# Kernel optimization log

Hardware: AMD Instinct MI355X
Metric: run time of the kernel (lower is better)

## Reference

```python
import jax, jax.numpy as jnp
import numpy as np

VOCAB = 30001  # vocab_size + 1
EMB = 64
CHAR = 50
RNN = 128
TAGS = 9
B, T = 256, 512
D_IN = EMB + CHAR  # 114


def lstm_scan(x, Wx, Wh, b):
    # x: [T, B, D]; Keras LSTM gate order i, f, g(c), o; sigmoid/tanh activations.
    Bsz = x.shape[1]
    H = Wh.shape[0]
    def step(carry, xt):
        h, c = carry
        z = xt @ Wx + h @ Wh + b  # [B, 4H]
        i, f, g, o = jnp.split(z, 4, axis=-1)
        c = jax.nn.sigmoid(f) * c + jax.nn.sigmoid(i) * jnp.tanh(g)
        h = jax.nn.sigmoid(o) * jnp.tanh(c)
        return (h, c), h
    init = (jnp.zeros((Bsz, H), x.dtype), jnp.zeros((Bsz, H), x.dtype))
    _, hs = jax.lax.scan(step, init, x)
    return hs  # [T, B, H]


def crf_log_likelihood(logits, labels, lengths, trans):
    # logits: [B,T,K]; labels: [B,T] int; lengths: [B] int; trans: [K,K]
    Bsz, Tlen, K = logits.shape
    mask = (jnp.arange(Tlen)[None, :] < lengths[:, None]).astype(logits.dtype)  # [B,T]
    # gold path score: unary + pairwise transition terms
    unary = jnp.take_along_axis(logits, labels[..., None], axis=-1)[..., 0]  # [B,T]
    unary_score = jnp.sum(unary * mask, axis=1)
    binary = trans[labels[:, :-1], labels[:, 1:]]  # [B,T-1]
    binary_score = jnp.sum(binary * mask[:, 1:], axis=1)
    seq_score = unary_score + binary_score
    # forward algorithm (log-domain scan over time)
    logits_t = jnp.transpose(logits, (1, 0, 2))  # [T,B,K]
    mask_t = jnp.transpose(mask[:, 1:])          # [T-1,B]
    def step(alpha, inp):
        logit_t, m = inp
        new = jax.nn.logsumexp(alpha[:, :, None] + trans[None], axis=1) + logit_t
        alpha = jnp.where(m[:, None] > 0, new, alpha)
        return alpha, None
    alpha, _ = jax.lax.scan(step, logits_t[0], (logits_t[1:], mask_t))
    log_norm = jax.nn.logsumexp(alpha, axis=1)
    log_norm = jnp.where(lengths > 0, log_norm, jnp.zeros_like(log_norm))
    return seq_score - log_norm


def setup_inputs() -> dict:
    key = jax.random.key(0)
    ks = jax.random.split(key, 12)
    inputs = jax.random.randint(ks[0], (B, T), 0, 30000, dtype=jnp.int32)
    char_embeddings = jax.random.normal(ks[1], (B, T, CHAR), dtype=jnp.float32)
    labels = jax.random.randint(ks[2], (B, T), 0, TAGS, dtype=jnp.int32)
    E = 0.1 * jax.random.normal(ks[3], (VOCAB, EMB), dtype=jnp.float32)
    s_in = 1.0 / np.sqrt(D_IN)
    s_h = 1.0 / np.sqrt(RNN)
    Wx_f = s_in * jax.random.normal(ks[4], (D_IN, 4 * RNN), dtype=jnp.float32)
    Wh_f = s_h * jax.random.normal(ks[5], (RNN, 4 * RNN), dtype=jnp.float32)
    b_f = jnp.zeros((4 * RNN,), jnp.float32)
    Wx_b = s_in * jax.random.normal(ks[6], (D_IN, 4 * RNN), dtype=jnp.float32)
    Wh_b = s_h * jax.random.normal(ks[7], (RNN, 4 * RNN), dtype=jnp.float32)
    b_b = jnp.zeros((4 * RNN,), jnp.float32)
    Wd = (1.0 / np.sqrt(2 * RNN)) * jax.random.normal(ks[8], (2 * RNN, TAGS), dtype=jnp.float32)
    bd = jnp.zeros((TAGS,), jnp.float32)
    transition = jax.random.uniform(ks[9], (TAGS, TAGS), dtype=jnp.float32)
    return {"inputs": inputs, "char_embeddings": char_embeddings, "labels": labels,
            "E": E, "Wx_f": Wx_f, "Wh_f": Wh_f, "b_f": b_f,
            "Wx_b": Wx_b, "Wh_b": Wh_b, "b_b": b_b,
            "Wd": Wd, "bd": bd, "transition": transition}


def reference(inputs, char_embeddings, labels, E, Wx_f, Wh_f, b_f, Wx_b, Wh_b, b_b, Wd, bd, transition):
    emb = E[inputs]                                      # [B,T,64]
    x = jnp.concatenate([emb, char_embeddings], axis=2)  # [B,T,114]
    xt = jnp.transpose(x, (1, 0, 2))                     # [T,B,114]
    h_f = lstm_scan(xt, Wx_f, Wh_f, b_f)                 # [T,B,128]
    h_b = lstm_scan(xt[::-1], Wx_b, Wh_b, b_b)[::-1]     # [T,B,128]
    out = jnp.concatenate([h_f, h_b], axis=-1)           # [T,B,256]
    logits = jnp.transpose(out, (1, 0, 2)) @ Wd + bd     # [B,T,9]
    lengths = jnp.sum((labels != 0).astype(jnp.int32), axis=1)
    log_likelihood = crf_log_likelihood(logits, labels, lengths, transition)
    return log_likelihood, transition
```

## Files before the change

kernel.cpp:

```cpp
#include <hip/hip_runtime.h>

#define BB   256
#define TT   512
#define EMBD 64
#define CHARD 50
#define DIN  114
#define RNN  128
#define NG   512
#define TAGS 9

typedef __bf16 bf16x8 __attribute__((ext_vector_type(8)));
typedef float  f32x4  __attribute__((ext_vector_type(4)));
typedef unsigned int u32x2 __attribute__((ext_vector_type(2)));

static __device__ __forceinline__ unsigned short f2bf(float f) {
  unsigned int u = __float_as_uint(f);
  unsigned int r = (u + 0x7FFFu + ((u >> 16) & 1u)) >> 16;
  return (unsigned short)r;
}
static __device__ __forceinline__ void gl_lds16(const void* g, void* l) {
  __builtin_amdgcn_global_load_lds(
      (const __attribute__((address_space(1))) unsigned int*)g,
      (__attribute__((address_space(3))) unsigned int*)l, 16, 0, 0);
}

__global__ void k_build_x(const int* __restrict__ inp, const float* __restrict__ ch,
                          const float* __restrict__ E, unsigned short* __restrict__ x) {
  int idx = blockIdx.x * 256 + threadIdx.x;
  int k   = idx & 127;
  int row = idx >> 7;
  float v;
  if (k < EMBD)      v = E[inp[row] * EMBD + k];
  else if (k < DIN)  v = ch[row * CHARD + (k - EMBD)];
  else               v = 0.f;
  x[idx] = f2bf(v);
}

__global__ void k_prep_w(const float* __restrict__ Wx_f, const float* __restrict__ Wh_f,
                         const float* __restrict__ Wx_b, const float* __restrict__ Wh_b,
                         const float* __restrict__ Wd,
                         unsigned short* __restrict__ WxT, unsigned short* __restrict__ WhT,
                         unsigned short* __restrict__ WdT) {
  if (blockIdx.x == 512) {
    for (int i = threadIdx.x; i < 16 * 256; i += 256) {
      int n = i >> 8, k = i & 255;
      WdT[i] = (n < TAGS) ? f2bf(Wd[k * TAGS + n]) : (unsigned short)0;
    }
    return;
  }
  int idx = blockIdx.x * 256 + threadIdx.x;
  int dir = idx >> 16;
  int rem = idx & 65535;
  int n   = rem >> 7;
  int kk  = rem & 127;
  const float* Wx = dir ? Wx_b : Wx_f;
  const float* Wh = dir ? Wh_b : Wh_f;
  WxT[idx] = (kk < DIN) ? f2bf(Wx[kk * NG + n]) : (unsigned short)0;
  WhT[idx] = f2bf(Wh[kk * NG + n]);
}

__global__ void k_lengths(const int* __restrict__ labels, int* __restrict__ lengths) {
  int b = blockIdx.x, lane = threadIdx.x;
  int cnt = 0;
  for (int t = lane; t < TT; t += 64) cnt += (labels[b * TT + t] != 0);
  for (int o = 32; o > 0; o >>= 1) cnt += __shfl_down(cnt, o);
  if (lane == 0) lengths[b] = cnt;
}

__global__ __launch_bounds__(512, 2) void k_fused(
    const unsigned short* __restrict__ x,
    const unsigned short* __restrict__ WxT,
    const unsigned short* __restrict__ WhT,
    const float* __restrict__ b_f, const float* __restrict__ b_b,
    const unsigned short* __restrict__ zcons, unsigned short* __restrict__ zprod,
    unsigned short* __restrict__ hseq, float* __restrict__ cbuf,
    int lstm_n, int s0, int s1, int first, int zs0, int znsteps)
{
  __shared__ __align__(16) char LDS[32768];
  const int tid = threadIdx.x, w = tid >> 6, l = tid & 63;
  const int lq = l & 15, lg = l >> 4;

  if ((int)blockIdx.x < lstm_n) {
    const int wg = blockIdx.x, dir = wg >> 5, rg = wg & 31, b0 = rg * 8;
    const unsigned short* WhD = WhT + dir * (NG * 128);
    unsigned short* hout = hseq + (size_t)dir * ((size_t)BB * TT * 128);
    char* ring = LDS;

    bf16x8 wh[4][4];
    #pragma unroll
    for (int g = 0; g < 4; ++g)
      #pragma unroll
      for (int kt = 0; kt < 4; ++kt)
        wh[g][kt] = *reinterpret_cast<const bf16x8*>(
            WhD + (g * RNN + w * 16 + lq) * 128 + kt * 32 + lg * 8);

    const int row7 = l & 7;
    int ro[4];
    #pragma unroll
    for (int kt = 0; kt < 4; ++kt)
      ro[kt] = (row7 * 16 + (((kt * 4) + lg) ^ row7)) * 16;

    int wo[2], rowr[2];
    #pragma unroll
    for (int rr = 0; rr < 2; ++rr) {
      rowr[rr] = (lg & 1) * 4 + (lg >> 1) * 2 + rr;
      int unit = rowr[rr] * 16 + ((w * 2 + (lq >> 3)) ^ rowr[rr]);
      wo[rr] = unit * 16 + (lq & 7) * 2;
    }
    const int hidden = w * 16 + lq;

    if (tid < 128) {
      int row = tid >> 4, h16 = tid & 15;
      int unit = row * 16 + (h16 ^ row);
      if (first) {
        *reinterpret_cast<f32x4*>(ring + 7 * 2048 + unit * 16) = f32x4{0.f, 0.f, 0.f, 0.f};
      } else {
        int tprev = dir ? (TT - s0) : (s0 - 1);
        bf16x8 v = *reinterpret_cast<const bf16x8*>(
            hout + ((size_t)(b0 + row) * TT + tprev) * 128 + h16 * 8);
        *reinterpret_cast<bf16x8*>(ring + 7 * 2048 + unit * 16) = v;
      }
    }
    float c[2];
    #pragma unroll
    for (int rr = 0; rr < 2; ++rr)
      c[rr] = first ? 0.f : cbuf[(size_t)(dir * BB + b0 + rowr[rr]) * RNN + hidden];
    __syncthreads();

    const unsigned short* zQ = zcons +
        (size_t)(((dir * 32 + rg) * 8 + w) * 2 + (lg & 1)) * 256 + lq * 4;
    u32x2 zA[4], zB[4];
    if (lg < 2) {
      #pragma unroll
      for (int g = 0; g < 4; ++g) zA[g] = *reinterpret_cast<const u32x2*>(zQ + g * 64);
      const unsigned short* zp1 = zQ + (size_t)((s0 + 1 < s1) ? 1 : 0) * 262144;
      #pragma unroll
      for (int g = 0; g < 4; ++g) zB[g] = *reinterpret_cast<const u32x2*>(zp1 + g * 64);
    }

    auto gather = [&](int sp) {
      int h16 = tid & 15, tc = (tid >> 4) & 3, row = tid >> 6;
      int ss = sp + tc, t = dir ? (TT - 1 - ss) : ss;
      bf16x8 v = *reinterpret_cast<const bf16x8*>(
          ring + (ss & 7) * 2048 + (row * 16 + (h16 ^ row)) * 16);
      *reinterpret_cast<bf16x8*>(hout + ((size_t)(b0 + row) * TT + t) * 128 + h16 * 8) = v;
    };

    for (int s = s0; s < s1; ++s) {
      f32x4 acc[4];
      #pragma unroll
      for (int g = 0; g < 4; ++g) {
        unsigned int lo = zA[g][0], hi = zA[g][1];
        f32x4 zv = f32x4{__uint_as_float(lo << 16), __uint_as_float(lo & 0xffff0000u),
                         __uint_as_float(hi << 16), __uint_as_float(hi & 0xffff0000u)};
        acc[g] = (lg < 2) ? zv : f32x4{0.f, 0.f, 0.f, 0.f};
      }
      {
        #pragma unroll
        for (int g = 0; g < 4; ++g) zA[g] = zB[g];
        int sn = (s + 2 < s1) ? (s + 2) : (s1 - 1);
        if (lg < 2) {
          const unsigned short* zp = zQ + (size_t)(sn - s0) * 262144;
          #pragma unroll
          for (int g = 0; g < 4; ++g) zB[g] = *reinterpret_cast<const u32x2*>(zp + g * 64);
        }
      }

      const char* rb = ring + ((s - 1) & 7) * 2048;
      bf16x8 hf[4];
      #pragma unroll
      for (int kt = 0; kt < 4; ++kt)
        hf[kt] = *reinterpret_cast<const bf16x8*>(rb + ro[kt]);
      #pragma unroll
      for (int kt = 0; kt < 4; ++kt)
        #pragma unroll
        for (int g = 0; g < 4; ++g)
          acc[g] = __builtin_amdgcn_mfma_f32_16x16x32_bf16(hf[kt], wh[g][kt], acc[g], 0, 0, 0);

      if ((s & 3) == 0 && s > s0) gather(s - 4);

      float sw_[4][2];
      #pragma unroll
      for (int g = 0; g < 4; ++g)
        #pragma unroll
        for (int rr = 0; rr < 2; ++rr) {
          float d = acc[g][2 + rr], sv = acc[g][2 + rr];
          asm volatile("v_permlane32_swap_b32 %0, %1" : "+v"(d), "+v"(sv));
          sw_[g][rr] = d;
        }

      char* wslot = ring + (s & 7) * 2048;
      #pragma unroll
      for (int rr = 0; rr < 2; ++rr) {
        float zi = (lg < 2) ? acc[0][rr] : sw_[0][rr];
        float zf = (lg < 2) ? acc[1][rr] : sw_[1][rr];
        float zg = (lg < 2) ? acc[2][rr] : sw_[2][rr];
        float zo = (lg < 2) ? acc[3][rr] : sw_[3][rr];
        zi = fminf(20.f, fmaxf(-20.f, zi));
        zf = fminf(20.f, fmaxf(-20.f, zf));
        zg = fminf(20.f, fmaxf(-20.f, zg));
        zo = fminf(20.f, fmaxf(-20.f, zo));
        float ei = __expf(-zi), ef = __expf(-zf), eo = __expf(-zo);
        float g2 = __expf(2.f * zg);
        float P   = (1.f + ei) * (g2 + 1.f);
        float efp = 1.f + ef;
        float cn  = (c[rr] * P + efp * (g2 - 1.f)) * __builtin_amdgcn_rcpf(efp * P);
        c[rr] = cn;
        float cc = fminf(20.f, fmaxf(-20.f, cn));
        float ec = __expf(2.f * cc);
        float hn = (ec - 1.f) * __builtin_amdgcn_rcpf((1.f + eo) * (ec + 1.f));
        *reinterpret_cast<unsigned short*>(wslot + wo[rr]) = f2bf(hn);
      }
      __builtin_amdgcn_sched_barrier(0);
      asm volatile("s_waitcnt lgkmcnt(0)" ::: "memory");
      __builtin_amdgcn_s_barrier();
      __builtin_amdgcn_sched_barrier(0);
    }

    gather(s1 - 4);
    #pragma unroll
    for (int rr = 0; rr < 2; ++rr)
      cbuf[(size_t)(dir * BB + b0 + rowr[rr]) * RNN + hidden] = c[rr];
  } else {
    if (znsteps <= 0) return;
    const int TCHN = znsteps >> 4;
    const int zb = blockIdx.x - lstm_n;
    const int per = 16 * TCHN;
    const int dir = zb / per;
    const int rem = zb % per;
    const int rg2 = rem / TCHN, tch = rem % TCHN;
    const int b0p = rg2 * 16;
    const int sb  = zs0 + tch * 16;

    const unsigned short* WxD = WxT + dir * (NG * 128);
    const float* bias = dir ? b_b : b_f;
    unsigned short* xr = (unsigned short*)LDS;

    bf16x8 wx[4][4];
    float  bs[4];
    #pragma unroll
    for (int g = 0; g < 4; ++g) {
      int n = g * RNN + w * 16 + lq;
      bs[g] = bias[n];
      #pragma unroll
      for (int kt = 0; kt < 4; ++kt)
        wx[g][kt] = *reinterpret_cast<const bf16x8*>(WxD + n * 128 + kt * 32 + lg * 8);
    }

    auto stage = [&](int ci) {
      int buf = ci & 1;
      #pragma unroll
      for (int jj = 0; jj < 2; ++jj) {
        int idx = w * 2 + jj, sc = idx >> 2, kt = idx & 3;
        int s = sb + ci * 4 + sc;
        int t = dir ? (TT - 1 - s) : s;
        gl_lds16(x + ((size_t)(b0p + lq) * TT + t) * 128 + kt * 32 + lg * 8,
                 xr + buf * 8192 + sc * 2048 + kt * 512);
      }
    };

    stage(0);
    for (int ci = 0; ci < 4; ++ci) {
      __syncthreads();
      if (ci < 3) stage(ci + 1);
      int buf = ci & 1;
      #pragma unroll
      for (int sc = 0; sc < 4; ++sc) {
        int s = sb + ci * 4 + sc;
        bf16x8 xf[4];
        #pragma unroll
        for (int kt = 0; kt < 4; ++kt)
          xf[kt] = *reinterpret_cast<const bf16x8*>(xr + buf * 8192 + sc * 2048 + kt * 512 + l * 8);
        f32x4 acc[4];
        #pragma unroll
        for (int g = 0; g < 4; ++g) acc[g] = f32x4{bs[g], bs[g], bs[g], bs[g]};
        #pragma unroll
        for (int kt = 0; kt < 4; ++kt)
          #pragma unroll
          for (int g = 0; g < 4; ++g)
            acc[g] = __builtin_amdgcn_mfma_f32_16x16x32_bf16(xf[kt], wx[g][kt], acc[g], 0, 0, 0);
        unsigned short* zp = zprod + (size_t)(s - zs0) * 262144 +
            (size_t)(((dir * 32 + rg2 * 2 + (lg >> 1)) * 8 + w) * 2 + (lg & 1)) * 256 + lq * 4;
        #pragma unroll
        for (int g = 0; g < 4; ++g) {
          ushort4 v;
          v.x = f2bf(acc[g][0]); v.y = f2bf(acc[g][1]);
          v.z = f2bf(acc[g][2]); v.w = f2bf(acc[g][3]);
          *reinterpret_cast<ushort4*>(zp + g * 64) = v;
        }
      }
    }
  }
}

__global__ __launch_bounds__(256) void k_logits(const unsigned short* __restrict__ hseq,
                                                const unsigned short* __restrict__ WdT,
                                                const float* __restrict__ bd,
                                                float* __restrict__ logits,
                                                float* __restrict__ euk) {
  __shared__ __align__(16) unsigned short xt[2][16384];
  const int tid = threadIdx.x, wv = tid >> 6, l = tid & 63;
  const int lq = l & 15, lg = l >> 4;
  const size_t HS = (size_t)BB * TT * 128;

  bf16x8 wb[8];
  #pragma unroll
  for (int kt = 0; kt < 8; ++kt)
    wb[kt] = *reinterpret_cast<const bf16x8*>(WdT + lq * 256 + kt * 32 + lg * 8);
  float bdv = (lq < TAGS) ? bd[lq] : 0.f;

  auto stage = [&](int it, int buf) {
    int bt0 = blockIdx.x * 256 + it * 64;
    #pragma unroll
    for (int i = 0; i < 8; ++i) {
      int v = tid + i * 256;
      int g = v ^ ((v >> 5) & 7);
      int row = g >> 5, cu = g & 31;
      const unsigned short* src = (cu < 16)
          ? hseq + (size_t)(bt0 + row) * 128 + cu * 8
          : hseq + HS + (size_t)(bt0 + row) * 128 + (cu - 16) * 8;
      gl_lds16(src, &xt[buf][(i * 256 + wv * 64) * 8]);
    }
  };

  stage(0, 0);
  for (int it = 0; it < 4; ++it) {
    __syncthreads();
    if (it < 3) stage(it + 1, (it + 1) & 1);
    int buf = it & 1;
    int bt0 = blockIdx.x * 256 + it * 64;
    int r0 = wv * 16;
    bf16x8 af[8];
    #pragma unroll
    for (int kt = 0; kt < 8; ++kt) {
      int u = (r0 + lq) * 32 + kt * 4 + lg;
      af[kt] = *reinterpret_cast<const bf16x8*>(&xt[buf][(u ^ ((u >> 5) & 7)) * 8]);
    }
    f32x4 acc = f32x4{bdv, bdv, bdv, bdv};
    #pragma unroll
    for (int kt = 0; kt < 8; ++kt)
      acc = __builtin_amdgcn_mfma_f32_16x16x32_bf16(af[kt], wb[kt], acc, 0, 0, 0);
    float mr[4];
    #pragma unroll
    for (int r = 0; r < 4; ++r) {
      float v = (lq < TAGS) ? acc[r] : -1e30f;
      #pragma unroll
      for (int o = 1; o < 16; o <<= 1) v = fmaxf(v, __shfl_xor(v, o, 16));
      mr[r] = v;
    }
    #pragma unroll
    for (int r = 0; r < 4; ++r) {
      int rowi = bt0 + r0 + lg * 4 + r;
      if (lq < TAGS) logits[(size_t)rowi * TAGS + lq] = acc[r];
      if (lq < 12) {
        float val = (lq < TAGS) ? __expf(acc[r] - mr[r]) : ((lq == TAGS) ? mr[r] : 0.f);
        euk[(size_t)rowi * 12 + lq] = val;
      }
    }
  }
}

__global__ void k_score(const float* __restrict__ logits, const int* __restrict__ labels,
                        const int* __restrict__ lengths, const float* __restrict__ trans,
                        float* __restrict__ scbuf) {
  int b = blockIdx.x, lane = threadIdx.x;
  int len = lengths[b];
  const float* lg = logits + (size_t)b * TT * TAGS;
  const int*   lab = labels + b * TT;
  float sc = 0.f;
  for (int t = lane; t < TT; t += 64) {
    if (t < len) {
      sc += lg[t * TAGS + lab[t]];
      if (t >= 1) sc += trans[lab[t - 1] * TAGS + lab[t]];
    }
  }
  for (int o = 32; o > 0; o >>= 1) sc += __shfl_down(sc, o);
  if (lane == 0) scbuf[b] = sc;
}

__global__ __launch_bounds__(256, 1) void k_crf2(const float* __restrict__ euk,
                                                 const float* __restrict__ scbuf,
                                                 const int* __restrict__ lengths,
                                                 const float* __restrict__ trans,
                                                 float* __restrict__ out) {
  const int wv = threadIdx.x >> 6, lane = threadIdx.x & 63;
  const int b = blockIdx.x * 4 + wv;
  const float* ep = euk + (size_t)b * TT * 12;
  const int len = lengths[b];
  const int lim = (len < TT) ? len : TT;

  float Et[81];
  #pragma unroll
  for (int i = 0; i < 81; ++i) Et[i] = __expf(trans[i]);

  float P[81];
  float Ks = 0.f;
  int   E2 = 0;

  const int t0 = 1 + lane * 8;
  auto rec = [&](int t) { int tl = (t < TT) ? t : (TT - 1); return ep + (size_t)tl * 12; };

  const float* p0 = rec(t0);
  float4 A0 = *(const float4*)p0, A1 = *(const float4*)(p0 + 4), A2 = *(const float4*)(p0 + 8);
  const float* p1 = rec(t0 + 1);
  float4 B0 = *(const float4*)p1, B1 = *(const float4*)(p1 + 4), B2 = *(const float4*)(p1 + 8);

  {
    float eu[9] = {A0.x, A0.y, A0.z, A0.w, A1.x, A1.y, A1.z, A1.w, A2.x};
    bool upd = t0 < lim;
    #pragma unroll
    for (int i = 0; i < 9; ++i)
      #pragma unroll
      for (int j = 0; j < 9; ++j)
        P[i * 9 + j] = upd ? Et[i * 9 + j] * eu[j] : ((i == j) ? 1.f : 0.f);
    Ks += upd ? A2.y : 0.f;
    A0 = B0; A1 = B1; A2 = B2;
    const float* pn = rec(t0 + 2);
    B0 = *(const float4*)pn; B1 = *(const float4*)(pn + 4); B2 = *(const float4*)(pn + 8);
  }

  for (int s = 1; s < 8; ++s) {
    float eu[9] = {A0.x, A0.y, A0.z, A0.w, A1.x, A1.y, A1.z, A1.w, A2.x};
    float mt = A2.y;
    bool upd = (t0 + s) < lim;
    A0 = B0; A1 = B1; A2 = B2;
    const float* pn = rec(t0 + s + 2);
    B0 = *(const float4*)pn; B1 = *(const float4*)(pn + 4); B2 = *(const float4*)(pn + 8);
    #pragma unroll
    for (int i = 0; i < 9; ++i) {
      float tmp[9];
      #pragma unroll
      for (int j = 0; j < 9; ++j) {
        float a = P[i * 9 + 0] * Et[0 * 9 + j];
        #pragma unroll
        for (int k = 1; k < 9; ++k) a = fmaf(P[i * 9 + k], Et[k * 9 + j], a);
        tmp[j] = a * eu[j];
      }
      #pragma unroll
      for (int j = 0; j < 9; ++j) P[i * 9 + j] = upd ? tmp[j] : P[i * 9 + j];
    }
    Ks += upd ? mt : 0.f;
  }

  {
    float m = P[0];
    #pragma unroll
    for (int e = 1; e < 81; ++e) m = fmaxf(m, P[e]);
    int ex; frexpf(m, &ex);
    #pragma unroll
    for (int e = 0; e < 81; ++e) P[e] = ldexpf(P[e], -ex);
    E2 += ex;
  }

  for (int d = 0; d < 6; ++d) {
    int msk = 1 << d;
    float Q[81];
    #pragma unroll
    for (int e = 0; e < 81; ++e) Q[e] = __shfl_xor(P[e], msk);
    int   E2p = __shfl_xor(E2, msk);
    float Ksp = __shfl_xor(Ks, msk);
    bool late = (lane & msk) != 0;
    #pragma unroll
    for (int e = 0; e < 81; ++e) {
      float a = P[e], q = Q[e];
      P[e] = late ? q : a;
      Q[e] = late ? a : q;
    }
    #pragma unroll
    for (int i = 0; i < 9; ++i) {
      float tmp[9];
      #pragma unroll
      for (int j = 0; j < 9; ++j) {
        float a = P[i * 9 + 0] * Q[0 * 9 + j];
        #pragma unroll
        for (int k = 1; k < 9; ++k) a = fmaf(P[i * 9 + k], Q[k * 9 + j], a);
        tmp[j] = a;
      }
      #pragma unroll
      for (int j = 0; j < 9; ++j) P[i * 9 + j] = tmp[j];
    }
    E2 += E2p; Ks += Ksp;
    float m = P[0];
    #pragma unroll
    for (int e = 1; e < 81; ++e) m = fmaxf(m, P[e]);
    int ex; frexpf(m, &ex);
    #pragma unroll
    for (int e = 0; e < 81; ++e) P[e] = ldexpf(P[e], -ex);
    E2 += ex;
  }

  float4 z0 = *(const float4*)ep, z1 = *(const float4*)(ep + 4), z2 = *(const float4*)(ep + 8);
  float eu0[9] = {z0.x, z0.y, z0.z, z0.w, z1.x, z1.y, z1.z, z1.w, z2.x};
  float alpha[9];
  #pragma unroll
  for (int j = 0; j < 9; ++j) {
    float a = eu0[0] * P[0 * 9 + j];
    #pragma unroll
    for (int i = 1; i < 9; ++i) a = fmaf(eu0[i], P[i * 9 + j], a);
    alpha[j] = a;
  }
  float S = ((alpha[0] + alpha[1]) + (alpha[2] + alpha[3])) +
            ((alpha[4] + alpha[5]) + (alpha[6] + alpha[7])) + alpha[8];
  float ln = logf(S) + (float)E2 * 0.69314718056f + Ks + z2.y;
  if (lane == 0) out[b] = (len > 0) ? (scbuf[b] - ln) : 0.f;
}

__global__ void k_copy_trans(const float* __restrict__ trans, float* __restrict__ out) {
  int i = threadIdx.x;
  if (i < TAGS * TAGS) out[BB + i] = trans[i];
}

extern "C" void kernel_launch(void* const* d_in, const int* in_sizes, int n_in,
                              void* d_out, int out_size, void* d_ws, size_t ws_size,
                              hipStream_t stream) {
  const int*   inp    = (const int*)d_in[0];
  const float* ch     = (const float*)d_in[1];
  const int*   labels = (const int*)d_in[2];
  const float* E      = (const float*)d_in[3];
  const float* Wx_f   = (const float*)d_in[4];
  const float* Wh_f   = (const float*)d_in[5];
  const float* b_f    = (const float*)d_in[6];
  const float* Wx_b   = (const float*)d_in[7];
  const float* Wh_b   = (const float*)d_in[8];
  const float* b_b    = (const float*)d_in[9];
  const float* Wd     = (const float*)d_in[10];
  const float* bd     = (const float*)d_in[11];
  const float* trans  = (const float*)d_in[12];
  float* out = (float*)d_out;

  unsigned short* x    = (unsigned short*)d_ws;
  unsigned short* hseq = x + (size_t)BB * TT * 128;
  unsigned short* WxT  = hseq + (size_t)2 * BB * TT * 128;
  unsigned short* WhT  = WxT + 2 * NG * 128;
  unsigned short* WdT  = WhT + 2 * NG * 128;
  float* logits        = (float*)(WdT + 16 * 256);
  float* euk           = logits + (size_t)BB * TT * TAGS;
  float* cbuf          = euk + (size_t)BB * TT * 12;
  float* scbuf         = cbuf + (size_t)2 * BB * RNN;
  int*   lengths       = (int*)(scbuf + BB);
  unsigned short* zbuf = (unsigned short*)(lengths + 256);

  const size_t zoff = (size_t)((char*)zbuf - (char*)d_ws);
  int NP = 4;
  const int cands[4] = {4, 8, 16, 32};
  for (int i = 0; i < 4; ++i) {
    NP = cands[i];
    if (zoff + 2ull * (size_t)(TT / NP) * 524288ull <= ws_size) break;
  }
  const int L = TT / NP;
  const size_t zsl = (size_t)L * 262144;

  k_build_x<<<(BB * TT * 128) / 256, 256, 0, stream>>>(inp, ch, E, x);
  k_prep_w<<<513, 256, 0, stream>>>(Wx_f, Wh_f, Wx_b, Wh_b, Wd, WxT, WhT, WdT);
  k_lengths<<<BB, 64, 0, stream>>>(labels, lengths);

  k_fused<<<2 * 16 * (L / 16), 512, 0, stream>>>(x, WxT, WhT, b_f, b_b,
                                                 zbuf, zbuf, hseq, cbuf,
                                                 0, 0, 0, 1, 0, L);
  for (int p = 0; p < NP; ++p) {
    int nz = (p + 1 < NP) ? 2 * 16 * (L / 16) : 0;
    k_fused<<<64 + nz, 512, 0, stream>>>(
        x, WxT, WhT, b_f, b_b,
        zbuf + (size_t)(p & 1) * zsl,
        zbuf + (size_t)((p + 1) & 1) * zsl,
        hseq, cbuf,
        64, p * L, (p + 1) * L, (p == 0) ? 1 : 0, (p + 1) * L, nz ? L : 0);
  }

  k_logits<<<(BB * TT) / 256, 256, 0, stream>>>(hseq, WdT, bd, logits, euk);
  k_score<<<BB, 64, 0, stream>>>(logits, labels, lengths, trans, scbuf);
  k_crf2<<<BB / 4, 256, 0, stream>>>(euk, scbuf, lengths, trans, out);
  k_copy_trans<<<1, 128, 0, stream>>>(trans, out);
}
```

Baseline: 605.6 us.

## Add producer wavefronts that prefetch gate inputs into LDS and write hidden states

Grows the LSTM workgroup from 8 to 10 wavefronts. The two extra producer waves stage the precomputed input-projection gates into a double-buffered LDS region with global_load_lds, and they also copy hidden states from the LDS ring out to global memory. The 8 compute waves no longer issue global loads or stores in the serial recurrence loop and instead read gate inputs from LDS. In exchange the workgroup uses more LDS and registers, the producer waves must match the compute waves' barrier count every step, and the launch bounds change may cap registers per thread.

```diff
diff --git a/kernel.cpp b/kernel.cpp
--- a/kernel.cpp
+++ b/kernel.cpp
@@ -67,7 +67,7 @@
   if (lane == 0) lengths[b] = cnt;
 }
 
-__global__ __launch_bounds__(512, 2) void k_fused(
+__global__ __launch_bounds__(640, 5) void k_fused(
     const unsigned short* __restrict__ x,
     const unsigned short* __restrict__ WxT,
     const unsigned short* __restrict__ WhT,
@@ -76,7 +76,7 @@
     unsigned short* __restrict__ hseq, float* __restrict__ cbuf,
     int lstm_n, int s0, int s1, int first, int zs0, int znsteps)
 {
-  __shared__ __align__(16) char LDS[32768];
+  __shared__ __align__(16) char LDS[49152];
   const int tid = threadIdx.x, w = tid >> 6, l = tid & 63;
   const int lq = l & 15, lg = l >> 4;
 
@@ -85,29 +85,33 @@
     const unsigned short* WhD = WhT + dir * (NG * 128);
     unsigned short* hout = hseq + (size_t)dir * ((size_t)BB * TT * 128);
     char* ring = LDS;
+    char* zst  = LDS + 16384;
 
     bf16x8 wh[4][4];
-    #pragma unroll
-    for (int g = 0; g < 4; ++g)
+    int ro[4], wo[2], rowr[2], hidden = 0;
+    float c[2] = {0.f, 0.f};
+    if (w < 8) {
+      #pragma unroll
+      for (int g = 0; g < 4; ++g)
+        #pragma unroll
+        for (int kt = 0; kt < 4; ++kt)
+          wh[g][kt] = *reinterpret_cast<const bf16x8*>(
+              WhD + (g * RNN + w * 16 + lq) * 128 + kt * 32 + lg * 8);
+      const int row7 = l & 7;
       #pragma unroll
       for (int kt = 0; kt < 4; ++kt)
-        wh[g][kt] = *reinterpret_cast<const bf16x8*>(
-            WhD + (g * RNN + w * 16 + lq) * 128 + kt * 32 + lg * 8);
-
-    const int row7 = l & 7;
-    int ro[4];
-    #pragma unroll
-    for (int kt = 0; kt < 4; ++kt)
-      ro[kt] = (row7 * 16 + (((kt * 4) + lg) ^ row7)) * 16;
-
-    int wo[2], rowr[2];
-    #pragma unroll
-    for (int rr = 0; rr < 2; ++rr) {
-      rowr[rr] = (lg & 1) * 4 + (lg >> 1) * 2 + rr;
-      int unit = rowr[rr] * 16 + ((w * 2 + (lq >> 3)) ^ rowr[rr]);
-      wo[rr] = unit * 16 + (lq & 7) * 2;
-    }
-    const int hidden = w * 16 + lq;
+        ro[kt] = (row7 * 16 + (((kt * 4) + lg) ^ row7)) * 16;
+      #pragma unroll
+      for (int rr = 0; rr < 2; ++rr) {
+        rowr[rr] = (lg & 1) * 4 + (lg >> 1) * 2 + rr;
+        int unit = rowr[rr] * 16 + ((w * 2 + (lq >> 3)) ^ rowr[rr]);
+        wo[rr] = unit * 16 + (lq & 7) * 2;
+      }
+      hidden = w * 16 + lq;
+      #pragma unroll
+      for (int rr = 0; rr < 2; ++rr)
+        c[rr] = first ? 0.f : cbuf[(size_t)(dir * BB + b0 + rowr[rr]) * RNN + hidden];
+    }
 
     if (tid < 128) {
       int row = tid >> 4, h16 = tid & 15;
@@ -121,106 +125,128 @@
         *reinterpret_cast<bf16x8*>(ring + 7 * 2048 + unit * 16) = v;
       }
     }
-    float c[2];
-    #pragma unroll
-    for (int rr = 0; rr < 2; ++rr)
-      c[rr] = first ? 0.f : cbuf[(size_t)(dir * BB + b0 + rowr[rr]) * RNN + hidden];
+
+    if (w >= 8) {
+      int sw = w - 8;
+      const unsigned short* src = zcons + (size_t)sw * 262144 + (size_t)(dir * 32 + rg) * 4096;
+      char* dst = zst + sw * 8192;
+      #pragma unroll
+      for (int i = 0; i < 8; ++i)
+        gl_lds16(src + i * 512 + l * 8, dst + i * 1024 + l * 16);
+      asm volatile("s_waitcnt vmcnt(0)" ::: "memory");
+    }
     __syncthreads();
 
-    const unsigned short* zQ = zcons +
-        (size_t)(((dir * 32 + rg) * 8 + w) * 2 + (lg & 1)) * 256 + lq * 4;
-    u32x2 zA[4], zB[4];
-    if (lg < 2) {
-      #pragma unroll
-      for (int g = 0; g < 4; ++g) zA[g] = *reinterpret_cast<const u32x2*>(zQ + g * 64);
-      const unsigned short* zp1 = zQ + (size_t)((s0 + 1 < s1) ? 1 : 0) * 262144;
-      #pragma unroll
-      for (int g = 0; g < 4; ++g) zB[g] = *reinterpret_cast<const u32x2*>(zp1 + g * 64);
-    }
-
-    auto gather = [&](int sp) {
-      int h16 = tid & 15, tc = (tid >> 4) & 3, row = tid >> 6;
-      int ss = sp + tc, t = dir ? (TT - 1 - ss) : ss;
-      bf16x8 v = *reinterpret_cast<const bf16x8*>(
-          ring + (ss & 7) * 2048 + (row * 16 + (h16 ^ row)) * 16);
-      *reinterpret_cast<bf16x8*>(hout + ((size_t)(b0 + row) * TT + t) * 128 + h16 * 8) = v;
-    };
-
-    for (int s = s0; s < s1; ++s) {
-      f32x4 acc[4];
-      #pragma unroll
-      for (int g = 0; g < 4; ++g) {
-        unsigned int lo = zA[g][0], hi = zA[g][1];
-        f32x4 zv = f32x4{__uint_as_float(lo << 16), __uint_as_float(lo & 0xffff0000u),
-                         __uint_as_float(hi << 16), __uint_as_float(hi & 0xffff0000u)};
-        acc[g] = (lg < 2) ? zv : f32x4{0.f, 0.f, 0.f, 0.f};
+    if (w < 8) {
+      for (int s = s0; s < s1; ++s) {
+        int ls = s - s0;
+        const char* zls = zst + ((ls >> 1) & 1) * 16384 + (ls & 1) * 8192 +
+                          (w * 2 + (lg & 1)) * 512 + lq * 8;
+        u32x2 zr[4];
+        #pragma unroll
+        for (int g = 0; g < 4; ++g)
+          zr[g] = *reinterpret_cast<const u32x2*>(zls + g * 128);
+
+        f32x4 acc[4];
+        #pragma unroll
+        for (int g = 0; g < 4; ++g) {
+          unsigned int lo = zr[g][0], hi = zr[g][1];
+          f32x4 zv = f32x4{__uint_as_float(lo << 16), __uint_as_float(lo & 0xffff0000u),
+                           __uint_as_float(hi << 16), __uint_as_float(hi & 0xffff0000u)};
+          acc[g] = (lg < 2) ? zv : f32x4{0.f, 0.f, 0.f, 0.f};
+        }
+
+        const char* rb = ring + ((s - 1) & 7) * 2048;
+        bf16x8 hf[4];
+        #pragma unroll
+        for (int kt = 0; kt < 4; ++kt)
+          hf[kt] = *reinterpret_cast<const bf16x8*>(rb + ro[kt]);
+        #pragma unroll
+        for (int kt = 0; kt < 4; ++kt)
+          #pragma unroll
+          for (int g = 0; g < 4; ++g)
+            acc[g] = __builtin_amdgcn_mfma_f32_16x16x32_bf16(hf[kt], wh[g][kt], acc[g], 0, 0, 0);
+
+        float sw_[4][2];
+        #pragma unroll
+        for (int g = 0; g < 4; ++g)
+          #pragma unroll
+          for (int rr = 0; rr < 2; ++rr) {
+            float d = acc[g][2 + rr], sv = acc[g][2 + rr];
+            asm volatile("v_permlane32_swap_b32 %0, %1" : "+v"(d), "+v"(sv));
+            sw_[g][rr] = d;
+          }
+
+        char* wslot = ring + (s & 7) * 2048;
+        #pragma unroll
+        for (int rr = 0; rr < 2; ++rr) {
+          float zi = (lg < 2) ? acc[0][rr] : sw_[0][rr];
+          float zf = (lg < 2) ? acc[1][rr] : sw_[1][rr];
+          float zg = (lg < 2) ? acc[2][rr] : sw_[2][rr];
+          float zo = (lg < 2) ? acc[3][rr] : sw_[3][rr];
+          zi = fminf(20.f, fmaxf(-20.f, zi));
+          zf = fminf(20.f, fmaxf(-20.f, zf));
+          zg = fminf(20.f, fmaxf(-20.f, zg));
+          zo = fminf(20.f, fmaxf(-20.f, zo));
+          float ei = __expf(-zi), ef = __expf(-zf), eo = __expf(-zo);
+          float g2 = __expf(2.f * zg);
+          float P   = (1.f + ei) * (g2 + 1.f);
+          float efp = 1.f + ef;
+          float cn  = (c[rr] * P + efp * (g2 - 1.f)) * __builtin_amdgcn_rcpf(efp * P);
+          c[rr] = cn;
+          float cc = fminf(20.f, fmaxf(-20.f, cn));
+          float ec = __expf(2.f * cc);
+          float hn = (ec - 1.f) * __builtin_amdgcn_rcpf((1.f + eo) * (ec + 1.f));
+          *reinterpret_cast<unsigned short*>(wslot + wo[rr]) = f2bf(hn);
+        }
+        __builtin_amdgcn_sched_barrier(0);
+        asm volatile("s_waitcnt lgkmcnt(0)" ::: "memory");
+        __builtin_amdgcn_s_barrier();
+        __builtin_amdgcn_sched_barrier(0);
+      }
+      #pragma unroll
+      for (int rr = 0; rr < 2; ++rr)
+        cbuf[(size_t)(dir * BB + b0 + rowr[rr]) * RNN + hidden] = c[rr];
+    } else {
+      const int sw = w - 8;
+      for (int s = s0; s < s1; ++s) {
+        int ls = s - s0;
+        if ((ls & 1) == 0 && s + 2 < s1) {
+          int st = ls + 2 + sw;
+          const unsigned short* src = zcons + (size_t)st * 262144 + (size_t)(dir * 32 + rg) * 4096;
+          char* dst = zst + (((ls >> 1) + 1) & 1) * 16384 + sw * 8192;
+          #pragma unroll
+          for (int i = 0; i < 8; ++i)
+            gl_lds16(src + i * 512 + l * 8, dst + i * 1024 + l * 16);
+        }
+        if ((s & 3) == 0 && s > s0) {
+          int lid = sw * 64 + l;
+          #pragma unroll
+          for (int j = 0; j < 4; ++j) {
+            int u = lid + j * 128;
+            int h16 = u & 15, tc = (u >> 4) & 3, row = u >> 6;
+            int ss = s - 4 + tc, t = dir ? (TT - 1 - ss) : ss;
+            bf16x8 v = *reinterpret_cast<const bf16x8*>(
+                ring + (ss & 7) * 2048 + (row * 16 + (h16 ^ row)) * 16);
+            *reinterpret_cast<bf16x8*>(hout + ((size_t)(b0 + row) * TT + t) * 128 + h16 * 8) = v;
+          }
+        }
+        if ((ls & 1) == 1) asm volatile("s_waitcnt vmcnt(0)" ::: "memory");
+        __builtin_amdgcn_s_barrier();
       }
       {
-        #pragma unroll
-        for (int g = 0; g < 4; ++g) zA[g] = zB[g];
-        int sn = (s + 2 < s1) ? (s + 2) : (s1 - 1);
-        if (lg < 2) {
-          const unsigned short* zp = zQ + (size_t)(sn - s0) * 262144;
-          #pragma unroll
-          for (int g = 0; g < 4; ++g) zB[g] = *reinterpret_cast<const u32x2*>(zp + g * 64);
+        int lid = sw * 64 + l;
+        #pragma unroll
+        for (int j = 0; j < 4; ++j) {
+          int u = lid + j * 128;
+          int h16 = u & 15, tc = (u >> 4) & 3, row = u >> 6;
+          int ss = s1 - 4 + tc, t = dir ? (TT - 1 - ss) : ss;
+          bf16x8 v = *reinterpret_cast<const bf16x8*>(
+              ring + (ss & 7) * 2048 + (row * 16 + (h16 ^ row)) * 16);
+          *reinterpret_cast<bf16x8*>(hout + ((size_t)(b0 + row) * TT + t) * 128 + h16 * 8) = v;
         }
       }
-
-      const char* rb = ring + ((s - 1) & 7) * 2048;
-      bf16x8 hf[4];
-      #pragma unroll
-      for (int kt = 0; kt < 4; ++kt)
-        hf[kt] = *reinterpret_cast<const bf16x8*>(rb + ro[kt]);
-      #pragma unroll
-      for (int kt = 0; kt < 4; ++kt)
-        #pragma unroll
-        for (int g = 0; g < 4; ++g)
-          acc[g] = __builtin_amdgcn_mfma_f32_16x16x32_bf16(hf[kt], wh[g][kt], acc[g], 0, 0, 0);
-
-      if ((s & 3) == 0 && s > s0) gather(s - 4);
-
-      float sw_[4][2];
-      #pragma unroll
-      for (int g = 0; g < 4; ++g)
-        #pragma unroll
-        for (int rr = 0; rr < 2; ++rr) {
-          float d = acc[g][2 + rr], sv = acc[g][2 + rr];
-          asm volatile("v_permlane32_swap_b32 %0, %1" : "+v"(d), "+v"(sv));
-          sw_[g][rr] = d;
-        }
-
-      char* wslot = ring + (s & 7) * 2048;
-      #pragma unroll
-      for (int rr = 0; rr < 2; ++rr) {
-        float zi = (lg < 2) ? acc[0][rr] : sw_[0][rr];
-        float zf = (lg < 2) ? acc[1][rr] : sw_[1][rr];
-        float zg = (lg < 2) ? acc[2][rr] : sw_[2][rr];
-        float zo = (lg < 2) ? acc[3][rr] : sw_[3][rr];
-        zi = fminf(20.f, fmaxf(-20.f, zi));
-        zf = fminf(20.f, fmaxf(-20.f, zf));
-        zg = fminf(20.f, fmaxf(-20.f, zg));
-        zo = fminf(20.f, fmaxf(-20.f, zo));
-        float ei = __expf(-zi), ef = __expf(-zf), eo = __expf(-zo);
-        float g2 = __expf(2.f * zg);
-        float P   = (1.f + ei) * (g2 + 1.f);
-        float efp = 1.f + ef;
-        float cn  = (c[rr] * P + efp * (g2 - 1.f)) * __builtin_amdgcn_rcpf(efp * P);
-        c[rr] = cn;
-        float cc = fminf(20.f, fmaxf(-20.f, cn));
-        float ec = __expf(2.f * cc);
-        float hn = (ec - 1.f) * __builtin_amdgcn_rcpf((1.f + eo) * (ec + 1.f));
-        *reinterpret_cast<unsigned short*>(wslot + wo[rr]) = f2bf(hn);
-      }
-      __builtin_amdgcn_sched_barrier(0);
-      asm volatile("s_waitcnt lgkmcnt(0)" ::: "memory");
-      __builtin_amdgcn_s_barrier();
-      __builtin_amdgcn_sched_barrier(0);
-    }
-
-    gather(s1 - 4);
-    #pragma unroll
-    for (int rr = 0; rr < 2; ++rr)
-      cbuf[(size_t)(dir * BB + b0 + rowr[rr]) * RNN + hidden] = c[rr];
+    }
   } else {
     if (znsteps <= 0) return;
     const int TCHN = znsteps >> 4;
@@ -238,16 +264,19 @@
 
     bf16x8 wx[4][4];
     float  bs[4];
-    #pragma unroll
-    for (int g = 0; g < 4; ++g) {
-      int n = g * RNN + w * 16 + lq;
-      bs[g] = bias[n];
-      #pragma unroll
-      for (int kt = 0; kt < 4; ++kt)
-        wx[g][kt] = *reinterpret_cast<const bf16x8*>(WxD + n * 128 + kt * 32 + lg * 8);
+    if (w < 8) {
+      #pragma unroll
+      for (int g = 0; g < 4; ++g) {
+        int n = g * RNN + w * 16 + lq;
+        bs[g] = bias[n];
+        #pragma unroll
+        for (int kt = 0; kt < 4; ++kt)
+          wx[g][kt] = *reinterpret_cast<const bf16x8*>(WxD + n * 128 + kt * 32 + lg * 8);
+      }
     }
 
     auto stage = [&](int ci) {
+      if (w >= 8) return;
       int buf = ci & 1;
       #pragma unroll
       for (int jj = 0; jj < 2; ++jj) {
@@ -263,30 +292,32 @@
     for (int ci = 0; ci < 4; ++ci) {
       __syncthreads();
       if (ci < 3) stage(ci + 1);
-      int buf = ci & 1;
-      #pragma unroll
-      for (int sc = 0; sc < 4; ++sc) {
-        int s = sb + ci * 4 + sc;
-        bf16x8 xf[4];
-        #pragma unroll
-        for (int kt = 0; kt < 4; ++kt)
-          xf[kt] = *reinterpret_cast<const bf16x8*>(xr + buf * 8192 + sc * 2048 + kt * 512 + l * 8);
-        f32x4 acc[4];
-        #pragma unroll
-        for (int g = 0; g < 4; ++g) acc[g] = f32x4{bs[g], bs[g], bs[g], bs[g]};
-        #pragma unroll
-        for (int kt = 0; kt < 4; ++kt)
-          #pragma unroll
-          for (int g = 0; g < 4; ++g)
-            acc[g] = __builtin_amdgcn_mfma_f32_16x16x32_bf16(xf[kt], wx[g][kt], acc[g], 0, 0, 0);
-        unsigned short* zp = zprod + (size_t)(s - zs0) * 262144 +
-            (size_t)(((dir * 32 + rg2 * 2 + (lg >> 1)) * 8 + w) * 2 + (lg & 1)) * 256 + lq * 4;
-        #pragma unroll
-        for (int g = 0; g < 4; ++g) {
-          ushort4 v;
-          v.x = f2bf(acc[g][0]); v.y = f2bf(acc[g][1]);
-          v.z = f2bf(acc[g][2]); v.w = f2bf(acc[g][3]);
-          *reinterpret_cast<ushort4*>(zp + g * 64) = v;
+      if (w < 8) {
+        int buf = ci & 1;
+        #pragma unroll
+        for (int sc = 0; sc < 4; ++sc) {
+          int s = sb + ci * 4 + sc;
+          bf16x8 xf[4];
+          #pragma unroll
+          for (int kt = 0; kt < 4; ++kt)
+            xf[kt] = *reinterpret_cast<const bf16x8*>(xr + buf * 8192 + sc * 2048 + kt * 512 + l * 8);
+          f32x4 acc[4];
+          #pragma unroll
+          for (int g = 0; g < 4; ++g) acc[g] = f32x4{bs[g], bs[g], bs[g], bs[g]};
+          #pragma unroll
+          for (int kt = 0; kt < 4; ++kt)
+            #pragma unroll
+            for (int g = 0; g < 4; ++g)
+              acc[g] = __builtin_amdgcn_mfma_f32_16x16x32_bf16(xf[kt], wx[g][kt], acc[g], 0, 0, 0);
+          unsigned short* zp = zprod + (size_t)(s - zs0) * 262144 +
+              (size_t)(((dir * 32 + rg2 * 2 + (lg >> 1)) * 8 + w) * 2 + (lg & 1)) * 256 + lq * 4;
+          #pragma unroll
+          for (int g = 0; g < 4; ++g) {
+            ushort4 v;
+            v.x = f2bf(acc[g][0]); v.y = f2bf(acc[g][1]);
+            v.z = f2bf(acc[g][2]); v.w = f2bf(acc[g][3]);
+            *reinterpret_cast<ushort4*>(zp + g * 64) = v;
+          }
         }
       }
     }
@@ -554,12 +585,12 @@
   k_prep_w<<<513, 256, 0, stream>>>(Wx_f, Wh_f, Wx_b, Wh_b, Wd, WxT, WhT, WdT);
   k_lengths<<<BB, 64, 0, stream>>>(labels, lengths);
 
-  k_fused<<<2 * 16 * (L / 16), 512, 0, stream>>>(x, WxT, WhT, b_f, b_b,
+  k_fused<<<2 * 16 * (L / 16), 640, 0, stream>>>(x, WxT, WhT, b_f, b_b,
                                                  zbuf, zbuf, hseq, cbuf,
                                                  0, 0, 0, 1, 0, L);
   for (int p = 0; p < NP; ++p) {
     int nz = (p + 1 < NP) ? 2 * 16 * (L / 16) : 0;
-    k_fused<<<64 + nz, 512, 0, stream>>>(
+    k_fused<<<64 + nz, 640, 0, stream>>>(
         x, WxT, WhT, b_f, b_b,
         zbuf + (size_t)(p & 1) * zsl,
         zbuf + (size_t)((p + 1) & 1) * zsl,
```

Result: slower. 938.9 us (+55.0%).
